# Kernel tuning notes

Hardware: AMD Instinct MI355X
Metric: run time of the kernel (lower is better)

The kernel has to match this reference:

```python
import jax, jax.numpy as jnp
import numpy as np
import math

N_HEAD = 16
HEAD_DIM = 64
N_EMBD = N_HEAD * HEAD_DIM  # 1024


def _alibi_slopes(n_heads):
    def pow2(n):
        start = 2.0 ** (-2.0 ** (-(math.log2(n) - 3)))
        return [start * (start ** i) for i in range(n)]
    if n_heads & (n_heads - 1) == 0:
        s = pow2(n_heads)
    else:
        cp2 = 2 ** math.floor(math.log2(n_heads))
        s = pow2(cp2)
        extra_base = 2.0 ** (-2.0 ** (-(math.log2(2 * cp2) - 3)))
        s += [extra_base * (extra_base ** i) for i in range(n_heads - cp2)]
        s = s[:n_heads]
    return jnp.asarray(np.array(s, dtype=np.float32))


def setup_inputs() -> dict:
    key = jax.random.key(0)
    k1, k2, k3, k4 = jax.random.split(key, 4)
    B, T = 2, 2048
    x = jax.random.normal(k1, (B, T, N_EMBD), dtype=jnp.float32)
    # c_attn weight for q,k (use_v=True -> 2*n_embd outputs), no bias
    W_attn = jax.random.normal(k2, (N_EMBD, 2 * N_EMBD), dtype=jnp.float32) * 0.02
    v_tmp = jax.random.normal(k3, (N_HEAD, N_HEAD), dtype=jnp.float32) * 0.02
    proj_tmp = jax.random.normal(k4, (N_HEAD, N_HEAD), dtype=jnp.float32) * 0.02
    return {"x": x, "W_attn": W_attn, "v_tmp": v_tmp, "proj_tmp": proj_tmp}


def reference(x, W_attn, v_tmp, proj_tmp):
    B, T, C = x.shape
    H, D = N_HEAD, HEAD_DIM
    scale = 1.0 / math.sqrt(D)

    qk = x @ W_attn  # (B,T,2C)
    q, k = qk[..., :C], qk[..., C:]
    q = q.reshape(B, T, H, D).transpose(0, 2, 1, 3)  # (B,H,T,D)
    k = k.reshape(B, T, H, D).transpose(0, 2, 1, 3)

    # V via Kronecker-lifted matrix: x @ kron(v_tmp, I_D)
    # block structure => mix head channels: out[...,j,d] = sum_i x[...,i,d]*v_tmp[i,j]
    xh = x.reshape(B, T, H, D)
    v = jnp.einsum('btid,ij->btjd', xh, v_tmp)  # (B,T,H,D)

    scores = jnp.einsum('bhqd,bhkd->bhqk', q, k) * scale  # (B,H,T,T)

    # ALiBi bias + causal mask
    pos = jnp.arange(T, dtype=jnp.float32)
    rel = pos[None, :] - pos[:, None]  # (T,T), mem - ctx
    slopes = _alibi_slopes(H)
    bias = slopes[:, None, None] * rel[None, :, :]
    causal = pos[None, :] <= pos[:, None]
    bias = jnp.where(causal[None, :, :], bias, -jnp.inf)
    scores = scores + bias[None]

    att = jax.nn.softmax(scores, axis=-1)
    y = jnp.einsum('bhqk,bkhd->bqhd', att, v)  # (B,T,H,D)

    # output proj via kron(proj_tmp, I_D).T: out[...,i,d] = sum_j y[...,j,d]*proj_tmp[i,j]
    y = jnp.einsum('btjd,ij->btid', y, proj_tmp)
    return y.reshape(B, T, C)
```

## Files before the change

### kernel.cpp

```cpp
#include <hip/hip_runtime.h>

typedef __attribute__((ext_vector_type(8))) __bf16 bf16x8;
typedef __attribute__((ext_vector_type(8))) unsigned short u16x8;
typedef __attribute__((ext_vector_type(4))) float f32x4;
typedef __attribute__((ext_vector_type(4))) unsigned int u32x4;

#define LOG2E 1.4426950408889634f

#define GLDS16(gp, lp)                                                \
  __builtin_amdgcn_global_load_lds(                                   \
      (const __attribute__((address_space(1))) void*)(gp),            \
      (__attribute__((address_space(3))) void*)(lp), 16, 0, 0)

__device__ __forceinline__ unsigned short f2b(float f) {
  return __builtin_bit_cast(unsigned short, (__bf16)f);
}
__device__ __forceinline__ float b2f(unsigned short h) {
  return __uint_as_float(((unsigned)h) << 16);
}
__device__ __forceinline__ unsigned cvt_pk(float a, float b) {
  unsigned r;
  asm("v_cvt_pk_bf16_f32 %0, %1, %2" : "=v"(r) : "v"(a), "v"(b));
  return r;
}
__device__ __forceinline__ void swap32(unsigned& a, unsigned& b) {
  asm("v_permlane32_swap_b32 %0, %1" : "+v"(a), "+v"(b));
}
__device__ __forceinline__ void swap16(unsigned& a, unsigned& b) {
  asm("v_permlane16_swap_b32 %0, %1" : "+v"(a), "+v"(b));
}

__global__ __launch_bounds__(256) void k_pre(const float* __restrict__ x,
                                             const float* __restrict__ vt,
                                             const float* __restrict__ W,
                                             unsigned short* __restrict__ xb,
                                             unsigned short* __restrict__ vb,
                                             unsigned short* __restrict__ Wt) {
  if (blockIdx.x < 1024) {
    __shared__ float s_vt[256];
    s_vt[threadIdx.x] = vt[threadIdx.x];
    __syncthreads();
    int g = blockIdx.x * 256 + threadIdx.x;
    int bt = g >> 6, d = g & 63;
    const float* xp = x + (size_t)bt * 1024 + d;
    float xi[16];
#pragma unroll
    for (int i = 0; i < 16; ++i) xi[i] = xp[i * 64];
#pragma unroll
    for (int i = 0; i < 16; ++i) xb[(size_t)bt * 1024 + i * 64 + d] = f2b(xi[i]);
#pragma unroll
    for (int j = 0; j < 16; ++j) {
      float s = 0.f;
#pragma unroll
      for (int i = 0; i < 16; ++i) s += xi[i] * s_vt[i * 16 + j];
      vb[(size_t)bt * 1024 + j * 64 + d] = f2b(s);
    }
  } else {
    __shared__ unsigned short tile[64][65];
    int id2 = blockIdx.x - 1024;
    int n0 = (id2 & 31) * 64;
    int k0 = (id2 >> 5) * 64;
    int tx = threadIdx.x & 63, ty = threadIdx.x >> 6;
#pragma unroll
    for (int r = 0; r < 16; ++r) {
      int kk = ty * 16 + r;
      tile[kk][tx] = f2b(W[(size_t)(k0 + kk) * 2048 + n0 + tx]);
    }
    __syncthreads();
#pragma unroll
    for (int r = 0; r < 16; ++r) {
      int nn = ty * 16 + r;
      Wt[(size_t)(n0 + nn) * 1024 + k0 + tx] = tile[tx][nn];
    }
  }
}

__global__ __launch_bounds__(256) void k_mid(const unsigned short* __restrict__ A,
                                             const unsigned short* __restrict__ Bt,
                                             unsigned short* __restrict__ C,
                                             const unsigned short* __restrict__ vb,
                                             unsigned short* __restrict__ Vt) {
  if (blockIdx.x < 512) {
    __shared__ unsigned short As[128 * 32];
    __shared__ unsigned short Bs[128 * 32];
    const int K = 1024;
    int m0 = (blockIdx.x & 31) * 128;
    int n0 = (blockIdx.x >> 5) * 128;
    int tid = threadIdx.x;
    int w = tid >> 6, lane = tid & 63;
    int lq = lane & 15, lk8 = (lane >> 4) * 8;
    int wr = (w >> 1) * 64, wc = (w & 1) * 64;
    f32x4 acc[4][4];
#pragma unroll
    for (int i = 0; i < 4; ++i)
#pragma unroll
      for (int j = 0; j < 4; ++j)
#pragma unroll
        for (int r = 0; r < 4; ++r) acc[i][j][r] = 0.f;

    for (int kk = 0; kk < K; kk += 32) {
      __syncthreads();
#pragma unroll
      for (int i = 0; i < 2; ++i) {
        int c = tid + 256 * i;
        int row = c >> 2, col = (c & 3) * 8;
        GLDS16(A + (size_t)(m0 + row) * K + kk + col, As + c * 8);
        GLDS16(Bt + (size_t)(n0 + row) * K + kk + col, Bs + c * 8);
      }
      __syncthreads();
      bf16x8 af[4], bf[4];
#pragma unroll
      for (int i = 0; i < 4; ++i) af[i] = *(const bf16x8*)(As + (wr + i * 16 + lq) * 32 + lk8);
#pragma unroll
      for (int j = 0; j < 4; ++j) bf[j] = *(const bf16x8*)(Bs + (wc + j * 16 + lq) * 32 + lk8);
#pragma unroll
      for (int i = 0; i < 4; ++i)
#pragma unroll
        for (int j = 0; j < 4; ++j)
          acc[i][j] = __builtin_amdgcn_mfma_f32_16x16x32_bf16(af[i], bf[j], acc[i][j], 0, 0, 0);
    }
#pragma unroll
    for (int i = 0; i < 4; ++i)
#pragma unroll
      for (int j = 0; j < 4; ++j)
#pragma unroll
        for (int r = 0; r < 4; ++r) {
          int m = m0 + wr + i * 16 + (lane >> 4) * 4 + r;
          int n = n0 + wc + j * 16 + lq;
          C[(size_t)m * 2048 + n] = f2b(acc[i][j][r]);
        }
  } else {
    __shared__ unsigned short tile[64][65];
    int id2 = blockIdx.x - 512;
    int t0 = (id2 & 31) * 64;
    int c0 = ((id2 >> 5) & 15) * 64;
    int b = id2 >> 9;
    int tx = threadIdx.x & 63, ty = threadIdx.x >> 6;
#pragma unroll
    for (int r = 0; r < 16; ++r) {
      int tt = ty * 16 + r;
      tile[tt][tx] = vb[((size_t)b * 2048 + t0 + tt) * 1024 + c0 + tx];
    }
    __syncthreads();
#pragma unroll
    for (int r = 0; r < 16; ++r) {
      int cc = ty * 16 + r;
      Vt[((size_t)b * 1024 + c0 + cc) * 2048 + t0 + tx] = tile[tx][cc];
    }
  }
}

__global__ __launch_bounds__(256, 4) void k_flash(const unsigned short* __restrict__ qkb,
                                                  const unsigned short* __restrict__ Vt,
                                                  unsigned short* __restrict__ y) {
  __shared__ unsigned short Ks[2][2][64 * 32];
  __shared__ unsigned short Vs[2][2][64 * 32];
  int id = blockIdx.x;
  int xcd = id & 7, s = id >> 3;
  int grp = xcd + 8 * (s & 3);
  int qt = 31 - (s >> 2);
  int hd = grp & 15, b = grp >> 4;
  int tid = threadIdx.x;
  int w = tid >> 6, lane = tid & 63;
  int quad = lane >> 4, lq = lane & 15, lk8 = quad * 8;
  int xk8 = (quad ^ ((lq >> 1) & 3)) * 8;
  int qh = w >> 1, kh = w & 1;
  int rs = tid >> 2;
  int csw = ((tid & 3) ^ ((tid >> 3) & 3)) * 8;
  const size_t rowb = (size_t)b * 2048;
  const size_t vrow = ((size_t)b * 1024 + hd * 64 + rs) * 2048 + csw;
  const size_t krow = ((rowb + rs) << 11) + 1024 + hd * 64 + csw;

  float slope = exp2f(-0.5f * (float)(hd + 1));
  const float c1 = 0.125f * LOG2E;
  const float c2 = slope * LOG2E;
  const float c16 = 16.0f * c2;
  const float SHIFT = 16.0f;

  bf16x8 ones;
#pragma unroll
  for (int i = 0; i < 8; ++i) ones[i] = (__bf16)1.0f;

  int q0 = qt * 64;
  int qrow = q0 + qh * 32;
  bf16x8 qf[2][2];
#pragma unroll
  for (int qs2 = 0; qs2 < 2; ++qs2) {
    int qg = qrow + qs2 * 16 + lq;
    qf[qs2][0] = *(const bf16x8*)(qkb + ((rowb + qg) << 11) + hd * 64 + lk8);
    qf[qs2][1] = *(const bf16x8*)(qkb + ((rowb + qg) << 11) + hd * 64 + 32 + lk8);
  }
  int kq0 = kh * 32 + quad * 4 - qrow - lq;
  float base0[4];
#pragma unroll
  for (int r = 0; r < 4; ++r) base0[r] = c2 * (float)(kq0 + r) - SHIFT;

  f32x4 o[4][2];
  f32x4 o4[2];
#pragma unroll
  for (int r = 0; r < 4; ++r) { o4[0][r] = 0.f; o4[1][r] = 0.f; }
#pragma unroll
  for (int jj = 0; jj < 4; ++jj)
#pragma unroll
    for (int qs2 = 0; qs2 < 2; ++qs2)
#pragma unroll
      for (int r = 0; r < 4; ++r) o[jj][qs2][r] = 0.f;

  GLDS16(qkb + krow,      &Ks[0][0][rs * 32 + (tid & 3) * 8]);
  GLDS16(qkb + krow + 32, &Ks[0][1][rs * 32 + (tid & 3) * 8]);
  GLDS16(Vt + vrow,       &Vs[0][0][rs * 32 + (tid & 3) * 8]);
  GLDS16(Vt + vrow + 32,  &Vs[0][1][rs * 32 + (tid & 3) * 8]);
  __syncthreads();
  int cur = 0;

#pragma unroll 1
  for (int kt = 0; kt <= qt; ++kt) {
    int k0 = kt * 64;
    if (kt < qt) {
      size_t koff = (size_t)(k0 + 64);
      int nxt = cur ^ 1;
      GLDS16(qkb + krow + (koff << 11),      &Ks[nxt][0][rs * 32 + (tid & 3) * 8]);
      GLDS16(qkb + krow + (koff << 11) + 32, &Ks[nxt][1][rs * 32 + (tid & 3) * 8]);
      GLDS16(Vt + vrow + koff,               &Vs[nxt][0][rs * 32 + (tid & 3) * 8]);
      GLDS16(Vt + vrow + koff + 32,          &Vs[nxt][1][rs * 32 + (tid & 3) * 8]);
    }
    bf16x8 kc[2][2];
#pragma unroll
    for (int ks2 = 0; ks2 < 2; ++ks2) {
      u16x8 t0 = *(const u16x8*)(&Ks[cur][0][(kh * 32 + ks2 * 16 + lq) * 32 + xk8]);
      u16x8 t1 = *(const u16x8*)(&Ks[cur][1][(kh * 32 + ks2 * 16 + lq) * 32 + xk8]);
      kc[ks2][0] = __builtin_bit_cast(bf16x8, t0);
      kc[ks2][1] = __builtin_bit_cast(bf16x8, t1);
    }
    __builtin_amdgcn_s_setprio(1);
    f32x4 S[2][2];
#pragma unroll
    for (int ks2 = 0; ks2 < 2; ++ks2)
#pragma unroll
      for (int qs2 = 0; qs2 < 2; ++qs2) {
        f32x4 a;
#pragma unroll
        for (int r = 0; r < 4; ++r) a[r] = 0.f;
        a = __builtin_amdgcn_mfma_f32_16x16x32_bf16(kc[ks2][0], qf[qs2][0], a, 0, 0, 0);
        a = __builtin_amdgcn_mfma_f32_16x16x32_bf16(kc[ks2][1], qf[qs2][1], a, 0, 0, 0);
        S[ks2][qs2] = a;
      }
    __builtin_amdgcn_s_setprio(0);
    float bk = c2 * (float)k0;
    float p[2][2][4];
    if (kt == qt) {
#pragma unroll
      for (int ks2 = 0; ks2 < 2; ++ks2)
#pragma unroll
        for (int qs2 = 0; qs2 < 2; ++qs2)
#pragma unroll
          for (int r = 0; r < 4; ++r) {
            float v = S[ks2][qs2][r] * c1 + (base0[r] + bk + c16 * (float)(ks2 - qs2));
            v = (k0 + kq0 + (ks2 - qs2) * 16 + r <= 0) ? v : -1e30f;
            p[ks2][qs2][r] = exp2f(v);
          }
    } else {
#pragma unroll
      for (int ks2 = 0; ks2 < 2; ++ks2)
#pragma unroll
        for (int qs2 = 0; qs2 < 2; ++qs2)
#pragma unroll
          for (int r = 0; r < 4; ++r) {
            float v = S[ks2][qs2][r] * c1 + (base0[r] + bk + c16 * (float)(ks2 - qs2));
            p[ks2][qs2][r] = exp2f(v);
          }
    }
    unsigned pk[2][2][2];
#pragma unroll
    for (int ks2 = 0; ks2 < 2; ++ks2)
#pragma unroll
      for (int qs2 = 0; qs2 < 2; ++qs2) {
        pk[ks2][qs2][0] = cvt_pk(p[ks2][qs2][0], p[ks2][qs2][1]);
        pk[ks2][qs2][1] = cvt_pk(p[ks2][qs2][2], p[ks2][qs2][3]);
      }
    bf16x8 pf[2];
#pragma unroll
    for (int qs2 = 0; qs2 < 2; ++qs2) {
      unsigned a0 = pk[0][qs2][0], b0 = pk[1][qs2][0];
      swap32(a0, b0); swap16(a0, b0);
      unsigned a1 = pk[0][qs2][1], b1 = pk[1][qs2][1];
      swap32(a1, b1); swap16(a1, b1);
      u32x4 t; t[0] = a0; t[1] = a1; t[2] = b0; t[3] = b1;
      pf[qs2] = __builtin_bit_cast(bf16x8, t);
    }
    __builtin_amdgcn_s_setprio(1);
    o4[0] = __builtin_amdgcn_mfma_f32_16x16x32_bf16(ones, pf[0], o4[0], 0, 0, 0);
    o4[1] = __builtin_amdgcn_mfma_f32_16x16x32_bf16(ones, pf[1], o4[1], 0, 0, 0);
#pragma unroll
    for (int jj = 0; jj < 4; ++jj) {
      u16x8 v0 = *(const u16x8*)(&Vs[cur][kh][(jj * 16 + lq) * 32 + xk8]);
      bf16x8 vf = __builtin_bit_cast(bf16x8, v0);
      o[jj][0] = __builtin_amdgcn_mfma_f32_16x16x32_bf16(vf, pf[0], o[jj][0], 0, 0, 0);
      o[jj][1] = __builtin_amdgcn_mfma_f32_16x16x32_bf16(vf, pf[1], o[jj][1], 0, 0, 0);
    }
    __builtin_amdgcn_s_setprio(0);
    if (kt < qt) {
      __syncthreads();
      cur ^= 1;
    }
  }

  __syncthreads();
  float* red0 = (float*)&Ks[0][0][0];
  float* red1 = (float*)&Vs[0][0][0];
  float* red = (qh ? red1 : red0) + lane * 36;
  if (kh == 1) {
#pragma unroll
    for (int jj = 0; jj < 4; ++jj)
#pragma unroll
      for (int qs2 = 0; qs2 < 2; ++qs2)
#pragma unroll
        for (int r = 0; r < 4; ++r) red[(jj * 2 + qs2) * 4 + r] = o[jj][qs2][r];
    red[32] = o4[0][0];
    red[33] = o4[1][0];
  }
  __syncthreads();
  if (kh == 0) {
#pragma unroll
    for (int jj = 0; jj < 4; ++jj)
#pragma unroll
      for (int qs2 = 0; qs2 < 2; ++qs2)
#pragma unroll
        for (int r = 0; r < 4; ++r) o[jj][qs2][r] += red[(jj * 2 + qs2) * 4 + r];
    float inv0 = 1.0f / (o4[0][0] + red[32]);
    float inv1 = 1.0f / (o4[1][0] + red[33]);
#pragma unroll
    for (int qs2 = 0; qs2 < 2; ++qs2) {
      float inv = qs2 ? inv1 : inv0;
      size_t base = ((rowb + qrow + qs2 * 16 + lq) << 10) + hd * 64 + quad * 4;
#pragma unroll
      for (int jj = 0; jj < 4; ++jj) {
        ushort4 pk4;
        pk4.x = f2b(o[jj][qs2][0] * inv);
        pk4.y = f2b(o[jj][qs2][1] * inv);
        pk4.z = f2b(o[jj][qs2][2] * inv);
        pk4.w = f2b(o[jj][qs2][3] * inv);
        *(ushort4*)(y + base + jj * 16) = pk4;
      }
    }
  }
}

__global__ __launch_bounds__(256) void k_proj(const unsigned short* __restrict__ yb,
                                              const float* __restrict__ pt,
                                              float* __restrict__ out) {
  __shared__ float s_pt[256];
  s_pt[threadIdx.x] = pt[threadIdx.x];
  __syncthreads();
  int g = blockIdx.x * 256 + threadIdx.x;
  int bt = g >> 6, d = g & 63;
  float yj[16];
#pragma unroll
  for (int j = 0; j < 16; ++j) yj[j] = b2f(yb[(size_t)bt * 1024 + j * 64 + d]);
#pragma unroll
  for (int i = 0; i < 16; ++i) {
    float s = 0.f;
#pragma unroll
    for (int j = 0; j < 16; ++j) s += yj[j] * s_pt[i * 16 + j];
    out[(size_t)bt * 1024 + i * 64 + d] = s;
  }
}

extern "C" void kernel_launch(void* const* d_in, const int* in_sizes, int n_in,
                              void* d_out, int out_size, void* d_ws, size_t ws_size,
                              hipStream_t stream) {
  const float* x  = (const float*)d_in[0];
  const float* W  = (const float*)d_in[1];
  const float* vt = (const float*)d_in[2];
  const float* pt = (const float*)d_in[3];
  float* out = (float*)d_out;

  char* ws = (char*)d_ws;
  unsigned short* xb  = (unsigned short*)(ws);
  unsigned short* Wt  = (unsigned short*)(ws + (8u  << 20));
  unsigned short* qkb = (unsigned short*)(ws + (12u << 20));
  unsigned short* vb  = (unsigned short*)(ws + (28u << 20));
  unsigned short* Vtr = (unsigned short*)(ws + (36u << 20));
  unsigned short* yb  = xb;

  k_pre  <<<1536, 256, 0, stream>>>(x, vt, W, xb, vb, Wt);
  k_mid  <<<1536, 256, 0, stream>>>(xb, Wt, qkb, vb, Vtr);
  k_flash<<<1024, 256, 0, stream>>>(qkb, Vtr, yb);
  k_proj <<<1024, 256, 0, stream>>>(yb, pt, out);
}
```

Baseline: 151.2 us.

## Triple-buffer K/V tiles in flash attention with prefetch distance two

Expands the LDS K/V staging from double to triple buffering and issues global-to-LDS loads two tiles ahead. Synchronisation changes from a full __syncthreads to a partial vmcnt wait plus a raw s_barrier, so the loads for the next-next tile can remain in flight across the barrier. The goal is to hide global memory latency behind the compute loop. In exchange, LDS use per block rises from 32KB to 48KB, which may lower occupancy below the launch_bounds target of 4 blocks per CU, and the manual waitcnt counting has to match exactly how many loads are outstanding.

```diff
diff --git a/kernel.cpp b/kernel.cpp
--- a/kernel.cpp
+++ b/kernel.cpp
@@ -153,8 +153,8 @@
 __global__ __launch_bounds__(256, 4) void k_flash(const unsigned short* __restrict__ qkb,
                                                   const unsigned short* __restrict__ Vt,
                                                   unsigned short* __restrict__ y) {
-  __shared__ unsigned short Ks[2][2][64 * 32];
-  __shared__ unsigned short Vs[2][2][64 * 32];
+  __shared__ unsigned short Ks[3][2][64 * 32];
+  __shared__ unsigned short Vs[3][2][64 * 32];
   int id = blockIdx.x;
   int xcd = id & 7, s = id >> 3;
   int grp = xcd + 8 * (s & 3);
@@ -167,6 +167,7 @@
   int qh = w >> 1, kh = w & 1;
   int rs = tid >> 2;
   int csw = ((tid & 3) ^ ((tid >> 3) & 3)) * 8;
+  int ld = rs * 32 + (tid & 3) * 8;
   const size_t rowb = (size_t)b * 2048;
   const size_t vrow = ((size_t)b * 1024 + hd * 64 + rs) * 2048 + csw;
   const size_t krow = ((rowb + rs) << 11) + 1024 + hd * 64 + csw;
@@ -206,23 +207,34 @@
 #pragma unroll
       for (int r = 0; r < 4; ++r) o[jj][qs2][r] = 0.f;
 
-  GLDS16(qkb + krow,      &Ks[0][0][rs * 32 + (tid & 3) * 8]);
-  GLDS16(qkb + krow + 32, &Ks[0][1][rs * 32 + (tid & 3) * 8]);
-  GLDS16(Vt + vrow,       &Vs[0][0][rs * 32 + (tid & 3) * 8]);
-  GLDS16(Vt + vrow + 32,  &Vs[0][1][rs * 32 + (tid & 3) * 8]);
-  __syncthreads();
+  GLDS16(qkb + krow,      &Ks[0][0][ld]);
+  GLDS16(qkb + krow + 32, &Ks[0][1][ld]);
+  GLDS16(Vt + vrow,       &Vs[0][0][ld]);
+  GLDS16(Vt + vrow + 32,  &Vs[0][1][ld]);
+  if (qt >= 1) {
+    size_t koff = 64;
+    GLDS16(qkb + krow + (koff << 11),      &Ks[1][0][ld]);
+    GLDS16(qkb + krow + (koff << 11) + 32, &Ks[1][1][ld]);
+    GLDS16(Vt + vrow + koff,               &Vs[1][0][ld]);
+    GLDS16(Vt + vrow + koff + 32,          &Vs[1][1][ld]);
+    asm volatile("s_waitcnt vmcnt(4)" ::: "memory");
+  } else {
+    asm volatile("s_waitcnt vmcnt(0)" ::: "memory");
+  }
+  __builtin_amdgcn_s_barrier();
+  __builtin_amdgcn_sched_barrier(0);
   int cur = 0;
 
 #pragma unroll 1
   for (int kt = 0; kt <= qt; ++kt) {
     int k0 = kt * 64;
-    if (kt < qt) {
-      size_t koff = (size_t)(k0 + 64);
-      int nxt = cur ^ 1;
-      GLDS16(qkb + krow + (koff << 11),      &Ks[nxt][0][rs * 32 + (tid & 3) * 8]);
-      GLDS16(qkb + krow + (koff << 11) + 32, &Ks[nxt][1][rs * 32 + (tid & 3) * 8]);
-      GLDS16(Vt + vrow + koff,               &Vs[nxt][0][rs * 32 + (tid & 3) * 8]);
-      GLDS16(Vt + vrow + koff + 32,          &Vs[nxt][1][rs * 32 + (tid & 3) * 8]);
+    if (kt + 2 <= qt) {
+      int c2i = cur + 2; if (c2i >= 3) c2i -= 3;
+      size_t koff = (size_t)(k0 + 128);
+      GLDS16(qkb + krow + (koff << 11),      &Ks[c2i][0][ld]);
+      GLDS16(qkb + krow + (koff << 11) + 32, &Ks[c2i][1][ld]);
+      GLDS16(Vt + vrow + koff,               &Vs[c2i][0][ld]);
+      GLDS16(Vt + vrow + koff + 32,          &Vs[c2i][1][ld]);
     }
     bf16x8 kc[2][2];
 #pragma unroll
@@ -300,8 +312,11 @@
     }
     __builtin_amdgcn_s_setprio(0);
     if (kt < qt) {
-      __syncthreads();
-      cur ^= 1;
+      if (kt + 2 <= qt) asm volatile("s_waitcnt vmcnt(4)" ::: "memory");
+      else              asm volatile("s_waitcnt vmcnt(0)" ::: "memory");
+      __builtin_amdgcn_s_barrier();
+      __builtin_amdgcn_sched_barrier(0);
+      ++cur; if (cur == 3) cur = 0;
     }
   }
 
```

After: 151.9 us. Within noise of the previous version (+0.5%).
